# Kernel optimization log

Hardware: AMD Instinct MI355X
Metric: run time of the kernel (lower is better)

The kernel has to match this reference:

```python
import jax, jax.numpy as jnp
import numpy as np

N_HEADS = 16


def setup_inputs() -> dict:
    key = jax.random.key(0)
    ks = jax.random.split(key, 6)
    B, S, E = 2, 2048, 1024
    scale = 1.0 / np.sqrt(E)
    return {
        "X": jax.random.normal(ks[0], (B, S, E), dtype=jnp.float32),
        "Wq": jax.random.normal(ks[1], (E, E), dtype=jnp.float32) * scale,
        "Wk": jax.random.normal(ks[2], (E, E), dtype=jnp.float32) * scale,
        "Wv": jax.random.normal(ks[3], (E, E), dtype=jnp.float32) * scale,
        "Wp": jax.random.normal(ks[4], (E, E), dtype=jnp.float32) * scale,
        "bp": jnp.zeros((E,), dtype=jnp.float32),
    }


def reference(X, Wq, Wk, Wv, Wp, bp):
    B, S, E = X.shape
    H = N_HEADS
    dk = E // H
    # qkv projections (Linear with weight [out,in] -> x @ W.T), split heads
    q = (X @ Wq.T).reshape(B, S, H, dk).transpose(0, 2, 1, 3)  # [B,H,S,dk]
    k = (X @ Wk.T).reshape(B, S, H, dk).transpose(0, 2, 1, 3)
    v = (X @ Wv.T).reshape(B, S, H, dk).transpose(0, 2, 1, 3)
    scores = jnp.einsum('bhqd,bhkd->bhqk', q, k) / jnp.sqrt(jnp.asarray(dk, X.dtype))
    causal = jnp.tril(jnp.ones((S, S), dtype=bool))  # [S,S]
    scores = jnp.where(causal[None, None], scores, jnp.asarray(-jnp.inf, X.dtype))
    attn = jax.nn.softmax(scores, axis=-1)  # [B,H,S,S]
    y = jnp.einsum('bhqk,bhkd->bhqd', attn, v)  # [B,H,S,dk]
    y = y.transpose(0, 2, 1, 3).reshape(B, S, E)
    return y @ Wp.T + bp
```

## Files before the change

### kernel.cpp

```cpp
#include <hip/hip_runtime.h>

typedef unsigned short u16;
typedef __bf16 bf16x8 __attribute__((ext_vector_type(8)));
typedef float f32x4 __attribute__((ext_vector_type(4)));
typedef unsigned short u16x8 __attribute__((ext_vector_type(8)));
typedef unsigned short u16x4 __attribute__((ext_vector_type(4)));

union B8 { u16x8 u; bf16x8 b; };

#define MFMA_BF16(a, b, c) __builtin_amdgcn_mfma_f32_16x16x32_bf16((a), (b), (c), 0, 0, 0)

__device__ __forceinline__ u16 f2bf(float f) {
  unsigned x = __float_as_uint(f);
  unsigned r = x + 0x7fffu + ((x >> 16) & 1u);
  return (u16)(r >> 16);
}

__device__ __forceinline__ unsigned cvt_pk_bf16(float lo, float hi) {
  unsigned r;
  asm("v_cvt_pk_bf16_f32 %0, %1, %2" : "=v"(r) : "v"(lo), "v"(hi));
  return r;
}

__device__ __forceinline__ void gl2lds16(const void* g, void* l) {
  __builtin_amdgcn_global_load_lds(
      (const __attribute__((address_space(1))) void*)g,
      (__attribute__((address_space(3))) void*)l, 16, 0, 0);
}

__global__ __launch_bounds__(256) void cast5_kernel(
    const float* __restrict__ X, const float* __restrict__ Wq,
    const float* __restrict__ Wk, const float* __restrict__ Wv,
    const float* __restrict__ Wp, u16* __restrict__ Xb, u16* __restrict__ Wqb,
    u16* __restrict__ Wkb, u16* __restrict__ Wvb, u16* __restrict__ Wpb) {
  size_t i = ((size_t)blockIdx.x * 256 + threadIdx.x) * 4;
  const float* src;
  u16* dst;
  size_t off;
  if (i < 4194304) {
    src = X; dst = Xb; off = i;
  } else if (i < 5242880) {
    src = Wq; dst = Wqb; off = i - 4194304;
  } else if (i < 6291456) {
    src = Wk; dst = Wkb; off = i - 5242880;
  } else if (i < 7340032) {
    src = Wv; dst = Wvb; off = i - 6291456;
  } else {
    src = Wp; dst = Wpb; off = i - 7340032;
  }
  float4 v = *(const float4*)(src + off);
  u16x4 o;
  o[0] = f2bf(v.x); o[1] = f2bf(v.y); o[2] = f2bf(v.z); o[3] = f2bf(v.w);
  *(u16x4*)(dst + off) = o;
}

template <int N0>
__device__ __forceinline__ void mfma16(f32x4 (&acc)[8][4], B8 (&af)[8], B8& b0,
                                       B8& b1) {
  __builtin_amdgcn_s_setprio(1);
#pragma unroll
  for (int m = 0; m < 8; ++m) {
    acc[m][N0] = MFMA_BF16(af[m].b, b0.b, acc[m][N0]);
    acc[m][N0 + 1] = MFMA_BF16(af[m].b, b1.b, acc[m][N0 + 1]);
  }
  __builtin_amdgcn_s_setprio(0);
}

__global__ __launch_bounds__(512, 2) void gemm_qkv256(
    const u16* __restrict__ Xb, const u16* __restrict__ Wb,
    u16* __restrict__ Qb, u16* __restrict__ Kb, u16* __restrict__ Vt) {
  __shared__ __align__(16) u16 Al[2][2][256 * 32];
  __shared__ __align__(16) u16 Bl[2][2][256 * 32];

  int tid = threadIdx.x, lane = tid & 63, w = tid >> 6;
  int wr = w >> 2, wc = w & 3;
  int l16 = lane & 15, lg = lane >> 4;

  int bid = blockIdx.x;
  int swz = (bid & 7) * 24 + (bid >> 3);
  int bm = swz / 12, bn = swz % 12;

  const u16* Ag = Xb + (size_t)bm * 256 * 1024;
  const u16* Bg = Wb + (size_t)bn * 256 * 1024;

  int srow = w * 16 + (lane >> 2);
  int scol = lane & 3;

  auto stA = [&](int buf, int kh, int kt) {
#pragma unroll
    for (int p2 = 0; p2 < 2; ++p2) {
      int r = p2 * 128 + srow;
      int sl = scol ^ ((r >> 1) & 3);
      gl2lds16(Ag + (size_t)r * 1024 + kt * 64 + kh * 32 + sl * 8,
               (char*)&Al[buf][kh][0] + (size_t)(p2 * 128 + w * 16) * 64);
    }
  };
  auto stB = [&](int buf, int kh, int kt) {
#pragma unroll
    for (int p2 = 0; p2 < 2; ++p2) {
      int r = p2 * 128 + srow;
      int sl = scol ^ ((r >> 1) & 3);
      gl2lds16(Bg + (size_t)r * 1024 + kt * 64 + kh * 32 + sl * 8,
               (char*)&Bl[buf][kh][0] + (size_t)(p2 * 128 + w * 16) * 64);
    }
  };
  auto ldA = [&](int buf, int kk, B8 (&af)[8]) {
#pragma unroll
    for (int m = 0; m < 8; ++m) {
      int r = wr * 128 + m * 16 + l16;
      af[m].u = *(const u16x8*)((const char*)&Al[buf][kk][0] + r * 64 +
                                ((lg ^ ((r >> 1) & 3)) << 4));
    }
  };
  auto ldB = [&](int buf, int kk, int nf, B8& bf) {
    int r = wc * 64 + nf * 16 + l16;
    bf.u = *(const u16x8*)((const char*)&Bl[buf][kk][0] + r * 64 +
                           ((lg ^ ((r >> 1) & 3)) << 4));
  };

  f32x4 acc[8][4] = {};

  stA(0, 0, 0); stB(0, 0, 0);
  stA(0, 1, 0); stB(0, 1, 0);
  stA(1, 0, 1); stB(1, 0, 1);
  asm volatile("s_waitcnt vmcnt(8)" ::: "memory");
  __builtin_amdgcn_s_barrier();

  B8 af[8], b0, b1;
  for (int I = 0; I < 8; ++I) {
    int p = 2 * I;
    bool last = (I == 7);
    stA(1, 1, p + 1);
    ldA(0, 0, af); ldB(0, 0, 0, b0); ldB(0, 0, 1, b1);
    mfma16<0>(acc, af, b0, b1);
    stB(1, 1, p + 1);
    ldB(0, 0, 2, b0); ldB(0, 0, 3, b1);
    mfma16<2>(acc, af, b0, b1);
    if (last) asm volatile("s_waitcnt vmcnt(0)" ::: "memory");
    else      asm volatile("s_waitcnt vmcnt(8)" ::: "memory");
    __builtin_amdgcn_s_barrier();
    if (!last) stA(0, 0, p + 2);
    ldA(0, 1, af); ldB(0, 1, 0, b0); ldB(0, 1, 1, b1);
    mfma16<0>(acc, af, b0, b1);
    if (!last) stB(0, 0, p + 2);
    ldB(0, 1, 2, b0); ldB(0, 1, 3, b1);
    mfma16<2>(acc, af, b0, b1);
    if (last) asm volatile("s_waitcnt vmcnt(0)" ::: "memory");
    else      asm volatile("s_waitcnt vmcnt(8)" ::: "memory");
    __builtin_amdgcn_s_barrier();
    if (!last) stA(0, 1, p + 2);
    ldA(1, 0, af); ldB(1, 0, 0, b0); ldB(1, 0, 1, b1);
    mfma16<0>(acc, af, b0, b1);
    if (!last) stB(0, 1, p + 2);
    ldB(1, 0, 2, b0); ldB(1, 0, 3, b1);
    mfma16<2>(acc, af, b0, b1);
    if (last) asm volatile("s_waitcnt vmcnt(0)" ::: "memory");
    else      asm volatile("s_waitcnt vmcnt(8)" ::: "memory");
    __builtin_amdgcn_s_barrier();
    if (!last) stA(1, 0, p + 3);
    ldA(1, 1, af); ldB(1, 1, 0, b0); ldB(1, 1, 1, b1);
    mfma16<0>(acc, af, b0, b1);
    if (!last) stB(1, 0, p + 3);
    ldB(1, 1, 2, b0); ldB(1, 1, 3, b1);
    mfma16<2>(acc, af, b0, b1);
    if (!last) {
      asm volatile("s_waitcnt vmcnt(8)" ::: "memory");
      __builtin_amdgcn_s_barrier();
    }
  }

  const float QSCALE = 0.18033688011112042f;
#pragma unroll
  for (int m = 0; m < 8; ++m)
#pragma unroll
    for (int nf = 0; nf < 4; ++nf) {
      int colg = bn * 256 + wc * 64 + nf * 16 + l16;
      int rowg = bm * 256 + wr * 128 + m * 16 + lg * 4;
      if (bn < 4) {
#pragma unroll
        for (int j = 0; j < 4; ++j)
          Qb[(size_t)(rowg + j) * 1024 + colg] = f2bf(acc[m][nf][j] * QSCALE);
      } else if (bn < 8) {
#pragma unroll
        for (int j = 0; j < 4; ++j)
          Kb[(size_t)(rowg + j) * 1024 + (colg - 1024)] = f2bf(acc[m][nf][j]);
      } else {
        int cv = colg - 2048;
        int hh = cv >> 6, d = cv & 63;
        int bb = rowg >> 11, s0 = rowg & 2047;
        u16x4 pk;
#pragma unroll
        for (int j = 0; j < 4; ++j) pk[j] = f2bf(acc[m][nf][j]);
        *(u16x4*)(Vt + ((size_t)(bb * 16 + hh) * 64 + d) * 2048 + s0) = pk;
      }
    }
}

__device__ __forceinline__ void gemm_body(const u16* __restrict__ A,
                                          const u16* __restrict__ Bw,
                                          float* __restrict__ Cout,
                                          const float* __restrict__ bias,
                                          int bm, int bn, u16* Asm, u16* Bsm) {
  const int Kd = 1024, N = 1024;
  int tid = threadIdx.x;
  int lane = tid & 63, w = tid >> 6;
  int wr = w >> 1, wc = w & 1;
  int l16 = lane & 15, lg = lane >> 4;

  const u16* Abase = A + (size_t)bm * 128 * Kd;
  const u16* Bbase = Bw + (size_t)bn * 128 * Kd;

  f32x4 acc[4][4] = {};

  for (int kt = 0; kt < Kd / 64; ++kt) {
    int k0 = kt * 64;
#pragma unroll
    for (int i = 0; i < 4; ++i) {
      int uu = i * 256 + tid;
      int r = uu >> 3;
      int s = (uu & 7) ^ (r & 7);
      gl2lds16(Abase + (size_t)r * Kd + k0 + s * 8, Asm + i * 2048 + w * 512);
      gl2lds16(Bbase + (size_t)r * Kd + k0 + s * 8, Bsm + i * 2048 + w * 512);
    }
    asm volatile("s_waitcnt vmcnt(0)" ::: "memory");
    __syncthreads();

    B8 af[4][2], bfr[4][2];
#pragma unroll
    for (int mi = 0; mi < 4; ++mi)
#pragma unroll
      for (int kk = 0; kk < 2; ++kk) {
        int r = wr * 64 + mi * 16 + l16;
        int s = kk * 4 + lg;
        af[mi][kk].u = *(const u16x8*)((const char*)Asm + r * 128 + ((s ^ (r & 7)) << 4));
      }
#pragma unroll
    for (int ni = 0; ni < 4; ++ni)
#pragma unroll
      for (int kk = 0; kk < 2; ++kk) {
        int r = wc * 64 + ni * 16 + l16;
        int s = kk * 4 + lg;
        bfr[ni][kk].u = *(const u16x8*)((const char*)Bsm + r * 128 + ((s ^ (r & 7)) << 4));
      }
#pragma unroll
    for (int mi = 0; mi < 4; ++mi)
#pragma unroll
      for (int ni = 0; ni < 4; ++ni) {
        acc[mi][ni] = MFMA_BF16(af[mi][0].b, bfr[ni][0].b, acc[mi][ni]);
        acc[mi][ni] = MFMA_BF16(af[mi][1].b, bfr[ni][1].b, acc[mi][ni]);
      }
    __syncthreads();
  }

#pragma unroll
  for (int mi = 0; mi < 4; ++mi)
#pragma unroll
    for (int ni = 0; ni < 4; ++ni) {
      int col = bn * 128 + wc * 64 + ni * 16 + l16;
#pragma unroll
      for (int j = 0; j < 4; ++j) {
        int row = bm * 128 + wr * 64 + mi * 16 + lg * 4 + j;
        Cout[(size_t)row * N + col] = acc[mi][ni][j] + bias[col];
      }
    }
}

__global__ __launch_bounds__(256) void gemm_proj_kernel(
    const u16* __restrict__ Y1, const u16* __restrict__ Wpb,
    float* __restrict__ out, const float* __restrict__ bias) {
  __shared__ __align__(16) u16 Asm[128 * 64];
  __shared__ __align__(16) u16 Bsm[128 * 64];
  gemm_body(Y1, Wpb, out, bias, blockIdx.y, blockIdx.x, Asm, Bsm);
}

__global__ __launch_bounds__(256, 4) void attn_kernel(const u16* __restrict__ Q,
                                                      const u16* __restrict__ K,
                                                      const u16* __restrict__ Vt,
                                                      u16* __restrict__ Y) {
  __shared__ __align__(16) u16 Kl[2][64 * 64];
  __shared__ __align__(16) u16 Vl[2][64 * 64];
  __shared__ __align__(16) u16 Pl[4][16 * 64];

  const int E = 1024, S = 2048;
  int tid = threadIdx.x;
  int lane = tid & 63, w = tid >> 6;
  int l16 = lane & 15, lg = lane >> 4;
  int h7 = l16 & 7;

  int bid = blockIdx.x;
  int bh = bid & 31;
  int u = bid >> 5;
  int g = u & 7, kq = u >> 3;
  int qt = (kq == 0) ? 31 - g : (kq == 1) ? 16 + g : (kq == 2) ? 15 - g : g;
  int b = bh >> 4, h = bh & 15;

  const u16* Qb = Q + (size_t)b * S * E + (size_t)h * 64;
  const u16* Kb = K + (size_t)b * S * E + (size_t)h * 64;
  const u16* Vb = Vt + (size_t)bh * 64 * 2048;

  int r0 = tid >> 3;
  int s0 = (tid & 7) ^ (r0 & 7);
  size_t koff = (size_t)r0 * 1024 + s0 * 8;
  size_t voff = (size_t)r0 * 2048 + s0 * 8;
  const u16* kpA = Kb;
  const u16* kpB = Kb + 32 * 1024;
  const u16* vpA = Vb;
  const u16* vpB = Vb + 32 * 2048;

  const char* kbase0 = (const char*)&Kl[0][0] + l16 * 128 + ((lg ^ h7) << 4);
  const char* kbase1 = (const char*)&Kl[0][0] + l16 * 128 + (((4 + lg) ^ h7) << 4);
  const char* vbase0 = (const char*)&Vl[0][0] + l16 * 128 + ((lg ^ h7) << 4);
  const char* vbase1 = (const char*)&Vl[0][0] + l16 * 128 + (((4 + lg) ^ h7) << 4);
  char* pw0 = (char*)&Pl[w][0] + l16 * 128 + (((0 * 2 + (lg >> 1)) ^ h7) << 4) + (lg & 1) * 8;
  char* pw1 = (char*)&Pl[w][0] + l16 * 128 + (((1 * 2 + (lg >> 1)) ^ h7) << 4) + (lg & 1) * 8;
  char* pw2 = (char*)&Pl[w][0] + l16 * 128 + (((2 * 2 + (lg >> 1)) ^ h7) << 4) + (lg & 1) * 8;
  char* pw3 = (char*)&Pl[w][0] + l16 * 128 + (((3 * 2 + (lg >> 1)) ^ h7) << 4) + (lg & 1) * 8;
  const char* pr0 = (const char*)&Pl[w][0] + l16 * 128 + ((lg ^ h7) << 4);
  const char* pr1 = (const char*)&Pl[w][0] + l16 * 128 + (((4 + lg) ^ h7) << 4);

  B8 qa[2];
#pragma unroll
  for (int kk = 0; kk < 2; ++kk)
    qa[kk].u = *(const u16x8*)(Qb + (size_t)(qt * 64 + w * 16 + l16) * E + kk * 32 + lg * 8);

  f32x4 o[4] = {};
  float lrun = 0.f;
  int qrow = w * 16 + l16;

  gl2lds16(kpA + koff, &Kl[0][w * 512]);
  gl2lds16(vpA + voff, &Vl[0][w * 512]);
  gl2lds16(kpB + koff, &Kl[0][2048 + w * 512]);
  gl2lds16(vpB + voff, &Vl[0][2048 + w * 512]);
  kpA += 65536; kpB += 65536; vpA += 64; vpB += 64;

#define ATTN_ITER(BF, DOMASK, DOSTAGE)                                         \
  do {                                                                         \
    asm volatile("s_waitcnt vmcnt(0)" ::: "memory");                           \
    __syncthreads();                                                           \
    if (DOSTAGE) {                                                             \
      gl2lds16(kpA + koff, &Kl[(BF) ^ 1][w * 512]);                            \
      gl2lds16(vpA + voff, &Vl[(BF) ^ 1][w * 512]);                            \
      gl2lds16(kpB + koff, &Kl[(BF) ^ 1][2048 + w * 512]);                     \
      gl2lds16(vpB + voff, &Vl[(BF) ^ 1][2048 + w * 512]);                     \
      kpA += 65536; kpB += 65536; vpA += 64; vpB += 64;                        \
    }                                                                          \
    f32x4 sa[4] = {};                                                          \
    __builtin_amdgcn_s_setprio(1);                                             \
    _Pragma("unroll") for (int nb = 0; nb < 4; ++nb) {                         \
      B8 kf0, kf1;                                                             \
      kf0.u = *(const u16x8*)(kbase0 + (BF)*8192 + nb * 2048);                 \
      kf1.u = *(const u16x8*)(kbase1 + (BF)*8192 + nb * 2048);                 \
      sa[nb] = MFMA_BF16(kf0.b, qa[0].b, sa[nb]);                              \
      sa[nb] = MFMA_BF16(kf1.b, qa[1].b, sa[nb]);                              \
    }                                                                          \
    __builtin_amdgcn_s_setprio(0);                                             \
    float p[16];                                                               \
    _Pragma("unroll") for (int nb = 0; nb < 4; ++nb)                           \
        _Pragma("unroll") for (int j = 0; j < 4; ++j) {                        \
      float pe = __builtin_amdgcn_exp2f(sa[nb][j]);                            \
      if (DOMASK) {                                                            \
        int kv = nb * 16 + lg * 4 + j;                                         \
        if (kv > qrow) pe = 0.f;                                               \
      }                                                                        \
      p[nb * 4 + j] = pe;                                                      \
    }                                                                          \
    {                                                                          \
      union { u16x4 v; unsigned uu[2]; } pk;                                   \
      pk.uu[0] = cvt_pk_bf16(p[0], p[1]);                                      \
      pk.uu[1] = cvt_pk_bf16(p[2], p[3]);                                      \
      *(u16x4*)pw0 = pk.v;                                                     \
      pk.uu[0] = cvt_pk_bf16(p[4], p[5]);                                      \
      pk.uu[1] = cvt_pk_bf16(p[6], p[7]);                                      \
      *(u16x4*)pw1 = pk.v;                                                     \
      pk.uu[0] = cvt_pk_bf16(p[8], p[9]);                                      \
      pk.uu[1] = cvt_pk_bf16(p[10], p[11]);                                    \
      *(u16x4*)pw2 = pk.v;                                                     \
      pk.uu[0] = cvt_pk_bf16(p[12], p[13]);                                    \
      pk.uu[1] = cvt_pk_bf16(p[14], p[15]);                                    \
      *(u16x4*)pw3 = pk.v;                                                     \
    }                                                                          \
    lrun += ((p[0] + p[1]) + (p[2] + p[3])) + ((p[4] + p[5]) + (p[6] + p[7])) +\
            ((p[8] + p[9]) + (p[10] + p[11])) +                                \
            ((p[12] + p[13]) + (p[14] + p[15]));                               \
    B8 pa0, pa1;                                                               \
    pa0.u = *(const u16x8*)pr0;                                                \
    pa1.u = *(const u16x8*)pr1;                                                \
    __builtin_amdgcn_s_setprio(1);                                             \
    _Pragma("unroll") for (int nb = 0; nb < 4; ++nb) {                         \
      B8 vf0, vf1;                                                             \
      vf0.u = *(const u16x8*)(vbase0 + (BF)*8192 + nb * 2048);                 \
      vf1.u = *(const u16x8*)(vbase1 + (BF)*8192 + nb * 2048);                 \
      o[nb] = MFMA_BF16(pa0.b, vf0.b, o[nb]);                                  \
      o[nb] = MFMA_BF16(pa1.b, vf1.b, o[nb]);                                  \
    }                                                                          \
    __builtin_amdgcn_s_setprio(0);                                             \
  } while (0)

  int U = qt;
  int i = 0;
  for (; i + 2 <= U; i += 2) {
    ATTN_ITER(0, false, true);
    ATTN_ITER(1, false, true);
  }
  if (U & 1) {
    ATTN_ITER(0, false, true);
    ATTN_ITER(1, true, false);
  } else {
    ATTN_ITER(0, true, false);
  }
#undef ATTN_ITER

  lrun += __shfl_xor(lrun, 16);
  lrun += __shfl_xor(lrun, 32);
  float inv[4];
#pragma unroll
  for (int j = 0; j < 4; ++j) {
    float lj = __shfl(lrun, (lane & 48) | (lg * 4 + j));
    inv[j] = 1.0f / lj;
  }
#pragma unroll
  for (int nb = 0; nb < 4; ++nb)
#pragma unroll
    for (int j = 0; j < 4; ++j) {
      int row = qt * 64 + w * 16 + lg * 4 + j;
      int col = h * 64 + nb * 16 + l16;
      Y[((size_t)b * S + row) * E + col] = f2bf(o[nb][j] * inv[j]);
    }
}

extern "C" void kernel_launch(void* const* d_in, const int* in_sizes, int n_in,
                              void* d_out, int out_size, void* d_ws,
                              size_t ws_size, hipStream_t stream) {
  const float* X = (const float*)d_in[0];
  const float* Wq = (const float*)d_in[1];
  const float* Wk = (const float*)d_in[2];
  const float* Wv = (const float*)d_in[3];
  const float* Wp = (const float*)d_in[4];
  const float* bp = (const float*)d_in[5];
  float* out = (float*)d_out;

  char* ws = (char*)d_ws;
  const size_t MB = 1ull << 20;
  u16* Xb = (u16*)(ws + 0 * MB);
  u16* Wqb = (u16*)(ws + 8 * MB);
  u16* Wkb = (u16*)(ws + 10 * MB);
  u16* Wvb = (u16*)(ws + 12 * MB);
  u16* Wpb = (u16*)(ws + 14 * MB);
  u16* Qb = (u16*)(ws + 16 * MB);
  u16* Kb = (u16*)(ws + 24 * MB);
  u16* VtB = (u16*)(ws + 32 * MB);
  u16* Y1 = (u16*)(ws + 40 * MB);

  cast5_kernel<<<8192, 256, 0, stream>>>(X, Wq, Wk, Wv, Wp, Xb, Wqb, Wkb, Wvb, Wpb);
  gemm_qkv256<<<192, 512, 0, stream>>>(Xb, Wqb, Qb, Kb, VtB);
  attn_kernel<<<1024, 256, 0, stream>>>(Qb, Kb, VtB, Y1);
  gemm_proj_kernel<<<dim3(8, 32), 256, 0, stream>>>(Y1, Wpb, out, bp);
}
```

Before: 104.1 us.

## Double query tile per attention block and double-buffer projection GEMM

The attention kernel now processes 128 query rows per block (32 per wave, two MFMA row groups), reusing each staged K/V tile for twice the queries and halving the grid to 512 blocks with occupancy hint lowered to 2. The causal tail handles two masked 64-key tiles with offsets. The projection GEMM gets double-buffered LDS staging with prefetch of the next K slice and raised MFMA priority, removing the trailing barrier. Risks include lower occupancy and coarser load balance across blocks.

```diff
diff --git a/kernel.cpp b/kernel.cpp
--- a/kernel.cpp
+++ b/kernel.cpp
@@ -196,34 +196,47 @@
     }
 }
 
-__device__ __forceinline__ void gemm_body(const u16* __restrict__ A,
-                                          const u16* __restrict__ Bw,
-                                          float* __restrict__ Cout,
-                                          const float* __restrict__ bias,
-                                          int bm, int bn, u16* Asm, u16* Bsm) {
+__global__ __launch_bounds__(256) void gemm_proj_kernel(
+    const u16* __restrict__ Y1, const u16* __restrict__ Wpb,
+    float* __restrict__ out, const float* __restrict__ bias) {
+  __shared__ __align__(16) u16 Asm[2][128 * 64];
+  __shared__ __align__(16) u16 Bsm[2][128 * 64];
+
   const int Kd = 1024, N = 1024;
+  int bm = blockIdx.y, bn = blockIdx.x;
   int tid = threadIdx.x;
   int lane = tid & 63, w = tid >> 6;
   int wr = w >> 1, wc = w & 1;
   int l16 = lane & 15, lg = lane >> 4;
 
-  const u16* Abase = A + (size_t)bm * 128 * Kd;
-  const u16* Bbase = Bw + (size_t)bn * 128 * Kd;
+  const u16* Abase = Y1 + (size_t)bm * 128 * Kd;
+  const u16* Bbase = Wpb + (size_t)bn * 128 * Kd;
+
+  int r0 = tid >> 3;
+  int s0 = (tid & 7) ^ (r0 & 7);
+
+  auto stage = [&](int buf, int kt) {
+#pragma unroll
+    for (int i = 0; i < 4; ++i) {
+      int r = i * 32 + r0;
+      int s = s0 ^ ((i & 3) == 0 ? 0 : 0);
+      (void)s;
+      int sl = (tid & 7) ^ (r & 7);
+      gl2lds16(Abase + (size_t)r * Kd + kt * 64 + sl * 8,
+               &Asm[buf][i * 2048 + w * 512]);
+      gl2lds16(Bbase + (size_t)r * Kd + kt * 64 + sl * 8,
+               &Bsm[buf][i * 2048 + w * 512]);
+    }
+  };
 
   f32x4 acc[4][4] = {};
-
-  for (int kt = 0; kt < Kd / 64; ++kt) {
-    int k0 = kt * 64;
-#pragma unroll
-    for (int i = 0; i < 4; ++i) {
-      int uu = i * 256 + tid;
-      int r = uu >> 3;
-      int s = (uu & 7) ^ (r & 7);
-      gl2lds16(Abase + (size_t)r * Kd + k0 + s * 8, Asm + i * 2048 + w * 512);
-      gl2lds16(Bbase + (size_t)r * Kd + k0 + s * 8, Bsm + i * 2048 + w * 512);
-    }
+  stage(0, 0);
+  int buf = 0;
+
+  for (int kt = 0; kt < 16; ++kt) {
     asm volatile("s_waitcnt vmcnt(0)" ::: "memory");
     __syncthreads();
+    if (kt + 1 < 16) stage(buf ^ 1, kt + 1);
 
     B8 af[4][2], bfr[4][2];
 #pragma unroll
@@ -232,7 +245,8 @@
       for (int kk = 0; kk < 2; ++kk) {
         int r = wr * 64 + mi * 16 + l16;
         int s = kk * 4 + lg;
-        af[mi][kk].u = *(const u16x8*)((const char*)Asm + r * 128 + ((s ^ (r & 7)) << 4));
+        af[mi][kk].u = *(const u16x8*)((const char*)&Asm[buf][0] + r * 128 +
+                                       ((s ^ (r & 7)) << 4));
       }
 #pragma unroll
     for (int ni = 0; ni < 4; ++ni)
@@ -240,8 +254,10 @@
       for (int kk = 0; kk < 2; ++kk) {
         int r = wc * 64 + ni * 16 + l16;
         int s = kk * 4 + lg;
-        bfr[ni][kk].u = *(const u16x8*)((const char*)Bsm + r * 128 + ((s ^ (r & 7)) << 4));
-      }
+        bfr[ni][kk].u = *(const u16x8*)((const char*)&Bsm[buf][0] + r * 128 +
+                                        ((s ^ (r & 7)) << 4));
+      }
+    __builtin_amdgcn_s_setprio(1);
 #pragma unroll
     for (int mi = 0; mi < 4; ++mi)
 #pragma unroll
@@ -249,7 +265,8 @@
         acc[mi][ni] = MFMA_BF16(af[mi][0].b, bfr[ni][0].b, acc[mi][ni]);
         acc[mi][ni] = MFMA_BF16(af[mi][1].b, bfr[ni][1].b, acc[mi][ni]);
       }
-    __syncthreads();
+    __builtin_amdgcn_s_setprio(0);
+    buf ^= 1;
   }
 
 #pragma unroll
@@ -260,26 +277,18 @@
 #pragma unroll
       for (int j = 0; j < 4; ++j) {
         int row = bm * 128 + wr * 64 + mi * 16 + lg * 4 + j;
-        Cout[(size_t)row * N + col] = acc[mi][ni][j] + bias[col];
-      }
-    }
-}
-
-__global__ __launch_bounds__(256) void gemm_proj_kernel(
-    const u16* __restrict__ Y1, const u16* __restrict__ Wpb,
-    float* __restrict__ out, const float* __restrict__ bias) {
-  __shared__ __align__(16) u16 Asm[128 * 64];
-  __shared__ __align__(16) u16 Bsm[128 * 64];
-  gemm_body(Y1, Wpb, out, bias, blockIdx.y, blockIdx.x, Asm, Bsm);
-}
-
-__global__ __launch_bounds__(256, 4) void attn_kernel(const u16* __restrict__ Q,
+        out[(size_t)row * N + col] = acc[mi][ni][j] + bias[col];
+      }
+    }
+}
+
+__global__ __launch_bounds__(256, 2) void attn_kernel(const u16* __restrict__ Q,
                                                       const u16* __restrict__ K,
                                                       const u16* __restrict__ Vt,
                                                       u16* __restrict__ Y) {
   __shared__ __align__(16) u16 Kl[2][64 * 64];
   __shared__ __align__(16) u16 Vl[2][64 * 64];
-  __shared__ __align__(16) u16 Pl[4][16 * 64];
+  __shared__ __align__(16) u16 Pl[4][32 * 64];
 
   const int E = 1024, S = 2048;
   int tid = threadIdx.x;
@@ -290,8 +299,7 @@
   int bid = blockIdx.x;
   int bh = bid & 31;
   int u = bid >> 5;
-  int g = u & 7, kq = u >> 3;
-  int qt = (kq == 0) ? 31 - g : (kq == 1) ? 16 + g : (kq == 2) ? 15 - g : g;
+  int qt = (u < 8) ? 15 - u : u - 8;
   int b = bh >> 4, h = bh & 15;
 
   const u16* Qb = Q + (size_t)b * S * E + (size_t)h * 64;
@@ -311,21 +319,23 @@
   const char* kbase1 = (const char*)&Kl[0][0] + l16 * 128 + (((4 + lg) ^ h7) << 4);
   const char* vbase0 = (const char*)&Vl[0][0] + l16 * 128 + ((lg ^ h7) << 4);
   const char* vbase1 = (const char*)&Vl[0][0] + l16 * 128 + (((4 + lg) ^ h7) << 4);
-  char* pw0 = (char*)&Pl[w][0] + l16 * 128 + (((0 * 2 + (lg >> 1)) ^ h7) << 4) + (lg & 1) * 8;
-  char* pw1 = (char*)&Pl[w][0] + l16 * 128 + (((1 * 2 + (lg >> 1)) ^ h7) << 4) + (lg & 1) * 8;
-  char* pw2 = (char*)&Pl[w][0] + l16 * 128 + (((2 * 2 + (lg >> 1)) ^ h7) << 4) + (lg & 1) * 8;
-  char* pw3 = (char*)&Pl[w][0] + l16 * 128 + (((3 * 2 + (lg >> 1)) ^ h7) << 4) + (lg & 1) * 8;
+  char* pw0 = (char*)&Pl[w][0] + l16 * 128 + (((0 + (lg >> 1)) ^ h7) << 4) + (lg & 1) * 8;
+  char* pw1 = (char*)&Pl[w][0] + l16 * 128 + (((2 + (lg >> 1)) ^ h7) << 4) + (lg & 1) * 8;
+  char* pw2 = (char*)&Pl[w][0] + l16 * 128 + (((4 + (lg >> 1)) ^ h7) << 4) + (lg & 1) * 8;
+  char* pw3 = (char*)&Pl[w][0] + l16 * 128 + (((6 + (lg >> 1)) ^ h7) << 4) + (lg & 1) * 8;
   const char* pr0 = (const char*)&Pl[w][0] + l16 * 128 + ((lg ^ h7) << 4);
   const char* pr1 = (const char*)&Pl[w][0] + l16 * 128 + (((4 + lg) ^ h7) << 4);
 
-  B8 qa[2];
-#pragma unroll
-  for (int kk = 0; kk < 2; ++kk)
-    qa[kk].u = *(const u16x8*)(Qb + (size_t)(qt * 64 + w * 16 + l16) * E + kk * 32 + lg * 8);
-
-  f32x4 o[4] = {};
-  float lrun = 0.f;
-  int qrow = w * 16 + l16;
+  B8 qa[2][2];
+#pragma unroll
+  for (int mi = 0; mi < 2; ++mi)
+#pragma unroll
+    for (int kk = 0; kk < 2; ++kk)
+      qa[mi][kk].u = *(const u16x8*)(Qb + (size_t)(qt * 128 + w * 32 + mi * 16 + l16) * E + kk * 32 + lg * 8);
+
+  f32x4 o[2][4] = {};
+  float lrun[2] = {0.f, 0.f};
+  int qloc = w * 32 + l16;
 
   gl2lds16(kpA + koff, &Kl[0][w * 512]);
   gl2lds16(vpA + voff, &Vl[0][w * 512]);
@@ -333,7 +343,7 @@
   gl2lds16(vpB + voff, &Vl[0][2048 + w * 512]);
   kpA += 65536; kpB += 65536; vpA += 64; vpB += 64;
 
-#define ATTN_ITER(BF, DOMASK, DOSTAGE)                                         \
+#define ATTN_ITER(BF, DOMASK, TOFF, DOSTAGE)                                   \
   do {                                                                         \
     asm volatile("s_waitcnt vmcnt(0)" ::: "memory");                           \
     __syncthreads();                                                           \
@@ -344,88 +354,94 @@
       gl2lds16(vpB + voff, &Vl[(BF) ^ 1][2048 + w * 512]);                     \
       kpA += 65536; kpB += 65536; vpA += 64; vpB += 64;                        \
     }                                                                          \
-    f32x4 sa[4] = {};                                                          \
+    f32x4 sa[2][4] = {};                                                       \
     __builtin_amdgcn_s_setprio(1);                                             \
     _Pragma("unroll") for (int nb = 0; nb < 4; ++nb) {                         \
       B8 kf0, kf1;                                                             \
-      kf0.u = *(const u16x8*)(kbase0 + (BF)*8192 + nb * 2048);                 \
-      kf1.u = *(const u16x8*)(kbase1 + (BF)*8192 + nb * 2048);                 \
-      sa[nb] = MFMA_BF16(kf0.b, qa[0].b, sa[nb]);                              \
-      sa[nb] = MFMA_BF16(kf1.b, qa[1].b, sa[nb]);                              \
+      kf0.u = *(const u16x8*)(kbase0 + (BF) * 8192 + nb * 2048);               \
+      kf1.u = *(const u16x8*)(kbase1 + (BF) * 8192 + nb * 2048);               \
+      sa[0][nb] = MFMA_BF16(kf0.b, qa[0][0].b, sa[0][nb]);                     \
+      sa[0][nb] = MFMA_BF16(kf1.b, qa[0][1].b, sa[0][nb]);                     \
+      sa[1][nb] = MFMA_BF16(kf0.b, qa[1][0].b, sa[1][nb]);                     \
+      sa[1][nb] = MFMA_BF16(kf1.b, qa[1][1].b, sa[1][nb]);                     \
     }                                                                          \
     __builtin_amdgcn_s_setprio(0);                                             \
-    float p[16];                                                               \
-    _Pragma("unroll") for (int nb = 0; nb < 4; ++nb)                           \
-        _Pragma("unroll") for (int j = 0; j < 4; ++j) {                        \
-      float pe = __builtin_amdgcn_exp2f(sa[nb][j]);                            \
-      if (DOMASK) {                                                            \
-        int kv = nb * 16 + lg * 4 + j;                                         \
-        if (kv > qrow) pe = 0.f;                                               \
+    _Pragma("unroll") for (int mi = 0; mi < 2; ++mi) {                         \
+      float p[16];                                                             \
+      _Pragma("unroll") for (int nb = 0; nb < 4; ++nb)                         \
+          _Pragma("unroll") for (int j = 0; j < 4; ++j) {                      \
+        float pe = __builtin_amdgcn_exp2f(sa[mi][nb][j]);                      \
+        if (DOMASK) {                                                          \
+          int kv = (TOFF) + nb * 16 + lg * 4 + j;                              \
+          if (kv > qloc + mi * 16) pe = 0.f;                                   \
+        }                                                                      \
+        p[nb * 4 + j] = pe;                                                    \
       }                                                                        \
-      p[nb * 4 + j] = pe;                                                      \
-    }                                                                          \
-    {                                                                          \
       union { u16x4 v; unsigned uu[2]; } pk;                                   \
       pk.uu[0] = cvt_pk_bf16(p[0], p[1]);                                      \
       pk.uu[1] = cvt_pk_bf16(p[2], p[3]);                                      \
-      *(u16x4*)pw0 = pk.v;                                                     \
+      *(u16x4*)(pw0 + mi * 2048) = pk.v;                                       \
       pk.uu[0] = cvt_pk_bf16(p[4], p[5]);                                      \
       pk.uu[1] = cvt_pk_bf16(p[6], p[7]);                                      \
-      *(u16x4*)pw1 = pk.v;                                                     \
+      *(u16x4*)(pw1 + mi * 2048) = pk.v;                                       \
       pk.uu[0] = cvt_pk_bf16(p[8], p[9]);                                      \
       pk.uu[1] = cvt_pk_bf16(p[10], p[11]);                                    \
-      *(u16x4*)pw2 = pk.v;                                                     \
+      *(u16x4*)(pw2 + mi * 2048) = pk.v;                                       \
       pk.uu[0] = cvt_pk_bf16(p[12], p[13]);                                    \
       pk.uu[1] = cvt_pk_bf16(p[14], p[15]);                                    \
-      *(u16x4*)pw3 = pk.v;                                                     \
+      *(u16x4*)(pw3 + mi * 2048) = pk.v;                                       \
+      lrun[mi] += ((p[0] + p[1]) + (p[2] + p[3])) +                            \
+                  ((p[4] + p[5]) + (p[6] + p[7])) +                            \
+                  ((p[8] + p[9]) + (p[10] + p[11])) +                          \
+                  ((p[12] + p[13]) + (p[14] + p[15]));                         \
     }                                                                          \
-    lrun += ((p[0] + p[1]) + (p[2] + p[3])) + ((p[4] + p[5]) + (p[6] + p[7])) +\
-            ((p[8] + p[9]) + (p[10] + p[11])) +                                \
-            ((p[12] + p[13]) + (p[14] + p[15]));                               \
-    B8 pa0, pa1;                                                               \
-    pa0.u = *(const u16x8*)pr0;                                                \
-    pa1.u = *(const u16x8*)pr1;                                                \
+    B8 pa00, pa01, pa10, pa11;                                                 \
+    pa00.u = *(const u16x8*)(pr0);                                             \
+    pa01.u = *(const u16x8*)(pr1);                                             \
+    pa10.u = *(const u16x8*)(pr0 + 2048);                                      \
+    pa11.u = *(const u16x8*)(pr1 + 2048);                                      \
     __builtin_amdgcn_s_setprio(1);                                             \
     _Pragma("unroll") for (int nb = 0; nb < 4; ++nb) {                         \
       B8 vf0, vf1;                                                             \
-      vf0.u = *(const u16x8*)(vbase0 + (BF)*8192 + nb * 2048);                 \
-      vf1.u = *(const u16x8*)(vbase1 + (BF)*8192 + nb * 2048);                 \
-      o[nb] = MFMA_BF16(pa0.b, vf0.b, o[nb]);                                  \
-      o[nb] = MFMA_BF16(pa1.b, vf1.b, o[nb]);                                  \
+      vf0.u = *(const u16x8*)(vbase0 + (BF) * 8192 + nb * 2048);               \
+      vf1.u = *(const u16x8*)(vbase1 + (BF) * 8192 + nb * 2048);               \
+      o[0][nb] = MFMA_BF16(pa00.b, vf0.b, o[0][nb]);                           \
+      o[0][nb] = MFMA_BF16(pa01.b, vf1.b, o[0][nb]);                           \
+      o[1][nb] = MFMA_BF16(pa10.b, vf0.b, o[1][nb]);                           \
+      o[1][nb] = MFMA_BF16(pa11.b, vf1.b, o[1][nb]);                           \
     }                                                                          \
     __builtin_amdgcn_s_setprio(0);                                             \
   } while (0)
 
-  int U = qt;
-  int i = 0;
-  for (; i + 2 <= U; i += 2) {
-    ATTN_ITER(0, false, true);
-    ATTN_ITER(1, false, true);
-  }
-  if (U & 1) {
-    ATTN_ITER(0, false, true);
-    ATTN_ITER(1, true, false);
-  } else {
-    ATTN_ITER(0, true, false);
-  }
+  int nt = 2 * qt;
+  for (int i = 0; i + 2 <= nt; i += 2) {
+    ATTN_ITER(0, false, 0, true);
+    ATTN_ITER(1, false, 0, true);
+  }
+  ATTN_ITER(0, true, 0, true);
+  ATTN_ITER(1, true, 64, false);
 #undef ATTN_ITER
 
-  lrun += __shfl_xor(lrun, 16);
-  lrun += __shfl_xor(lrun, 32);
-  float inv[4];
-#pragma unroll
-  for (int j = 0; j < 4; ++j) {
-    float lj = __shfl(lrun, (lane & 48) | (lg * 4 + j));
-    inv[j] = 1.0f / lj;
-  }
-#pragma unroll
-  for (int nb = 0; nb < 4; ++nb)
+#pragma unroll
+  for (int mi = 0; mi < 2; ++mi) {
+    float l = lrun[mi];
+    l += __shfl_xor(l, 16);
+    l += __shfl_xor(l, 32);
+    float inv[4];
 #pragma unroll
     for (int j = 0; j < 4; ++j) {
-      int row = qt * 64 + w * 16 + lg * 4 + j;
-      int col = h * 64 + nb * 16 + l16;
-      Y[((size_t)b * S + row) * E + col] = f2bf(o[nb][j] * inv[j]);
-    }
+      float lj = __shfl(l, (lane & 48) | (lg * 4 + j));
+      inv[j] = 1.0f / lj;
+    }
+#pragma unroll
+    for (int nb = 0; nb < 4; ++nb)
+#pragma unroll
+      for (int j = 0; j < 4; ++j) {
+        int row = qt * 128 + w * 32 + mi * 16 + lg * 4 + j;
+        int col = h * 64 + nb * 16 + l16;
+        Y[((size_t)b * S + row) * E + col] = f2bf(o[mi][nb][j] * inv[j]);
+      }
+  }
 }
 
 extern "C" void kernel_launch(void* const* d_in, const int* in_sizes, int n_in,
@@ -453,6 +469,6 @@
 
   cast5_kernel<<<8192, 256, 0, stream>>>(X, Wq, Wk, Wv, Wp, Xb, Wqb, Wkb, Wvb, Wpb);
   gemm_qkv256<<<192, 512, 0, stream>>>(Xb, Wqb, Qb, Kb, VtB);
-  attn_kernel<<<1024, 256, 0, stream>>>(Qb, Kb, VtB, Y1);
+  attn_kernel<<<512, 256, 0, stream>>>(Qb, Kb, VtB, Y1);
   gemm_proj_kernel<<<dim3(8, 32), 256, 0, stream>>>(Y1, Wpb, out, bp);
 }
```

Measured after the change: 109.7 us. 5.4% more time.

## Replace 256-tile QKV GEMM with double-buffered 128-tile kernel; double-buffer proj GEMM

Applied to the files above, without the earlier changes.

Swaps the hand-scheduled 256x256, 512-thread QKV GEMM for a 128x128, 256-thread kernel with a simple two-stage LDS double buffer and a swizzled 768-block grid. The projection GEMM gets the same double-buffered loop, which prefetches the next K tile while computing the current one and drops the trailing barrier. The aim is more blocks for better CU occupancy and load balance, plus overlap of global loads with MFMA. The cost is less data reuse per tile and more global traffic for the QKV GEMM.

```diff
diff --git a/kernel.cpp b/kernel.cpp
--- a/kernel.cpp
+++ b/kernel.cpp
@@ -54,176 +54,47 @@
   *(u16x4*)(dst + off) = o;
 }
 
-template <int N0>
-__device__ __forceinline__ void mfma16(f32x4 (&acc)[8][4], B8 (&af)[8], B8& b0,
-                                       B8& b1) {
-  __builtin_amdgcn_s_setprio(1);
-#pragma unroll
-  for (int m = 0; m < 8; ++m) {
-    acc[m][N0] = MFMA_BF16(af[m].b, b0.b, acc[m][N0]);
-    acc[m][N0 + 1] = MFMA_BF16(af[m].b, b1.b, acc[m][N0 + 1]);
-  }
-  __builtin_amdgcn_s_setprio(0);
-}
-
-__global__ __launch_bounds__(512, 2) void gemm_qkv256(
+__global__ __launch_bounds__(256, 2) void gemm_qkv128(
     const u16* __restrict__ Xb, const u16* __restrict__ Wb,
     u16* __restrict__ Qb, u16* __restrict__ Kb, u16* __restrict__ Vt) {
-  __shared__ __align__(16) u16 Al[2][2][256 * 32];
-  __shared__ __align__(16) u16 Bl[2][2][256 * 32];
-
-  int tid = threadIdx.x, lane = tid & 63, w = tid >> 6;
-  int wr = w >> 2, wc = w & 3;
-  int l16 = lane & 15, lg = lane >> 4;
-
-  int bid = blockIdx.x;
-  int swz = (bid & 7) * 24 + (bid >> 3);
-  int bm = swz / 12, bn = swz % 12;
-
-  const u16* Ag = Xb + (size_t)bm * 256 * 1024;
-  const u16* Bg = Wb + (size_t)bn * 256 * 1024;
-
-  int srow = w * 16 + (lane >> 2);
-  int scol = lane & 3;
-
-  auto stA = [&](int buf, int kh, int kt) {
-#pragma unroll
-    for (int p2 = 0; p2 < 2; ++p2) {
-      int r = p2 * 128 + srow;
-      int sl = scol ^ ((r >> 1) & 3);
-      gl2lds16(Ag + (size_t)r * 1024 + kt * 64 + kh * 32 + sl * 8,
-               (char*)&Al[buf][kh][0] + (size_t)(p2 * 128 + w * 16) * 64);
-    }
-  };
-  auto stB = [&](int buf, int kh, int kt) {
-#pragma unroll
-    for (int p2 = 0; p2 < 2; ++p2) {
-      int r = p2 * 128 + srow;
-      int sl = scol ^ ((r >> 1) & 3);
-      gl2lds16(Bg + (size_t)r * 1024 + kt * 64 + kh * 32 + sl * 8,
-               (char*)&Bl[buf][kh][0] + (size_t)(p2 * 128 + w * 16) * 64);
-    }
-  };
-  auto ldA = [&](int buf, int kk, B8 (&af)[8]) {
-#pragma unroll
-    for (int m = 0; m < 8; ++m) {
-      int r = wr * 128 + m * 16 + l16;
-      af[m].u = *(const u16x8*)((const char*)&Al[buf][kk][0] + r * 64 +
-                                ((lg ^ ((r >> 1) & 3)) << 4));
-    }
-  };
-  auto ldB = [&](int buf, int kk, int nf, B8& bf) {
-    int r = wc * 64 + nf * 16 + l16;
-    bf.u = *(const u16x8*)((const char*)&Bl[buf][kk][0] + r * 64 +
-                           ((lg ^ ((r >> 1) & 3)) << 4));
-  };
-
-  f32x4 acc[8][4] = {};
-
-  stA(0, 0, 0); stB(0, 0, 0);
-  stA(0, 1, 0); stB(0, 1, 0);
-  stA(1, 0, 1); stB(1, 0, 1);
-  asm volatile("s_waitcnt vmcnt(8)" ::: "memory");
-  __builtin_amdgcn_s_barrier();
-
-  B8 af[8], b0, b1;
-  for (int I = 0; I < 8; ++I) {
-    int p = 2 * I;
-    bool last = (I == 7);
-    stA(1, 1, p + 1);
-    ldA(0, 0, af); ldB(0, 0, 0, b0); ldB(0, 0, 1, b1);
-    mfma16<0>(acc, af, b0, b1);
-    stB(1, 1, p + 1);
-    ldB(0, 0, 2, b0); ldB(0, 0, 3, b1);
-    mfma16<2>(acc, af, b0, b1);
-    if (last) asm volatile("s_waitcnt vmcnt(0)" ::: "memory");
-    else      asm volatile("s_waitcnt vmcnt(8)" ::: "memory");
-    __builtin_amdgcn_s_barrier();
-    if (!last) stA(0, 0, p + 2);
-    ldA(0, 1, af); ldB(0, 1, 0, b0); ldB(0, 1, 1, b1);
-    mfma16<0>(acc, af, b0, b1);
-    if (!last) stB(0, 0, p + 2);
-    ldB(0, 1, 2, b0); ldB(0, 1, 3, b1);
-    mfma16<2>(acc, af, b0, b1);
-    if (last) asm volatile("s_waitcnt vmcnt(0)" ::: "memory");
-    else      asm volatile("s_waitcnt vmcnt(8)" ::: "memory");
-    __builtin_amdgcn_s_barrier();
-    if (!last) stA(0, 1, p + 2);
-    ldA(1, 0, af); ldB(1, 0, 0, b0); ldB(1, 0, 1, b1);
-    mfma16<0>(acc, af, b0, b1);
-    if (!last) stB(0, 1, p + 2);
-    ldB(1, 0, 2, b0); ldB(1, 0, 3, b1);
-    mfma16<2>(acc, af, b0, b1);
-    if (last) asm volatile("s_waitcnt vmcnt(0)" ::: "memory");
-    else      asm volatile("s_waitcnt vmcnt(8)" ::: "memory");
-    __builtin_amdgcn_s_barrier();
-    if (!last) stA(1, 0, p + 3);
-    ldA(1, 1, af); ldB(1, 1, 0, b0); ldB(1, 1, 1, b1);
-    mfma16<0>(acc, af, b0, b1);
-    if (!last) stB(1, 0, p + 3);
-    ldB(1, 1, 2, b0); ldB(1, 1, 3, b1);
-    mfma16<2>(acc, af, b0, b1);
-    if (!last) {
-      asm volatile("s_waitcnt vmcnt(8)" ::: "memory");
-      __builtin_amdgcn_s_barrier();
-    }
-  }
-
-  const float QSCALE = 0.18033688011112042f;
-#pragma unroll
-  for (int m = 0; m < 8; ++m)
-#pragma unroll
-    for (int nf = 0; nf < 4; ++nf) {
-      int colg = bn * 256 + wc * 64 + nf * 16 + l16;
-      int rowg = bm * 256 + wr * 128 + m * 16 + lg * 4;
-      if (bn < 4) {
-#pragma unroll
-        for (int j = 0; j < 4; ++j)
-          Qb[(size_t)(rowg + j) * 1024 + colg] = f2bf(acc[m][nf][j] * QSCALE);
-      } else if (bn < 8) {
-#pragma unroll
-        for (int j = 0; j < 4; ++j)
-          Kb[(size_t)(rowg + j) * 1024 + (colg - 1024)] = f2bf(acc[m][nf][j]);
-      } else {
-        int cv = colg - 2048;
-        int hh = cv >> 6, d = cv & 63;
-        int bb = rowg >> 11, s0 = rowg & 2047;
-        u16x4 pk;
-#pragma unroll
-        for (int j = 0; j < 4; ++j) pk[j] = f2bf(acc[m][nf][j]);
-        *(u16x4*)(Vt + ((size_t)(bb * 16 + hh) * 64 + d) * 2048 + s0) = pk;
-      }
-    }
-}
-
-__device__ __forceinline__ void gemm_body(const u16* __restrict__ A,
-                                          const u16* __restrict__ Bw,
-                                          float* __restrict__ Cout,
-                                          const float* __restrict__ bias,
-                                          int bm, int bn, u16* Asm, u16* Bsm) {
-  const int Kd = 1024, N = 1024;
+  __shared__ __align__(16) u16 Asm[2][128 * 64];
+  __shared__ __align__(16) u16 Bsm[2][128 * 64];
+
+  const int Kd = 1024;
   int tid = threadIdx.x;
   int lane = tid & 63, w = tid >> 6;
   int wr = w >> 1, wc = w & 1;
   int l16 = lane & 15, lg = lane >> 4;
 
-  const u16* Abase = A + (size_t)bm * 128 * Kd;
-  const u16* Bbase = Bw + (size_t)bn * 128 * Kd;
+  int bid = blockIdx.x;
+  int swz = (bid & 7) * 96 + (bid >> 3);
+  int bm = swz / 24, bn = swz % 24;
+
+  const u16* Abase = Xb + (size_t)bm * 128 * Kd;
+  const u16* Bbase = Wb + (size_t)bn * 128 * Kd;
+
+  int r0 = tid >> 3;
+
+  auto stage = [&](int buf, int kt) {
+#pragma unroll
+    for (int i = 0; i < 4; ++i) {
+      int r = i * 32 + r0;
+      int sl = (tid & 7) ^ (r & 7);
+      gl2lds16(Abase + (size_t)r * Kd + kt * 64 + sl * 8,
+               &Asm[buf][i * 2048 + w * 512]);
+      gl2lds16(Bbase + (size_t)r * Kd + kt * 64 + sl * 8,
+               &Bsm[buf][i * 2048 + w * 512]);
+    }
+  };
 
   f32x4 acc[4][4] = {};
-
-  for (int kt = 0; kt < Kd / 64; ++kt) {
-    int k0 = kt * 64;
-#pragma unroll
-    for (int i = 0; i < 4; ++i) {
-      int uu = i * 256 + tid;
-      int r = uu >> 3;
-      int s = (uu & 7) ^ (r & 7);
-      gl2lds16(Abase + (size_t)r * Kd + k0 + s * 8, Asm + i * 2048 + w * 512);
-      gl2lds16(Bbase + (size_t)r * Kd + k0 + s * 8, Bsm + i * 2048 + w * 512);
-    }
+  stage(0, 0);
+  int buf = 0;
+
+  for (int kt = 0; kt < 16; ++kt) {
     asm volatile("s_waitcnt vmcnt(0)" ::: "memory");
     __syncthreads();
+    if (kt + 1 < 16) stage(buf ^ 1, kt + 1);
 
     B8 af[4][2], bfr[4][2];
 #pragma unroll
@@ -232,7 +103,8 @@
       for (int kk = 0; kk < 2; ++kk) {
         int r = wr * 64 + mi * 16 + l16;
         int s = kk * 4 + lg;
-        af[mi][kk].u = *(const u16x8*)((const char*)Asm + r * 128 + ((s ^ (r & 7)) << 4));
+        af[mi][kk].u = *(const u16x8*)((const char*)&Asm[buf][0] + r * 128 +
+                                       ((s ^ (r & 7)) << 4));
       }
 #pragma unroll
     for (int ni = 0; ni < 4; ++ni)
@@ -240,8 +112,10 @@
       for (int kk = 0; kk < 2; ++kk) {
         int r = wc * 64 + ni * 16 + l16;
         int s = kk * 4 + lg;
-        bfr[ni][kk].u = *(const u16x8*)((const char*)Bsm + r * 128 + ((s ^ (r & 7)) << 4));
-      }
+        bfr[ni][kk].u = *(const u16x8*)((const char*)&Bsm[buf][0] + r * 128 +
+                                        ((s ^ (r & 7)) << 4));
+      }
+    __builtin_amdgcn_s_setprio(1);
 #pragma unroll
     for (int mi = 0; mi < 4; ++mi)
 #pragma unroll
@@ -249,18 +123,33 @@
         acc[mi][ni] = MFMA_BF16(af[mi][0].b, bfr[ni][0].b, acc[mi][ni]);
         acc[mi][ni] = MFMA_BF16(af[mi][1].b, bfr[ni][1].b, acc[mi][ni]);
       }
-    __syncthreads();
-  }
-
+    __builtin_amdgcn_s_setprio(0);
+    buf ^= 1;
+  }
+
+  const float QSCALE = 0.18033688011112042f;
 #pragma unroll
   for (int mi = 0; mi < 4; ++mi)
 #pragma unroll
     for (int ni = 0; ni < 4; ++ni) {
-      int col = bn * 128 + wc * 64 + ni * 16 + l16;
-#pragma unroll
-      for (int j = 0; j < 4; ++j) {
-        int row = bm * 128 + wr * 64 + mi * 16 + lg * 4 + j;
-        Cout[(size_t)row * N + col] = acc[mi][ni][j] + bias[col];
+      int colg = bn * 128 + wc * 64 + ni * 16 + l16;
+      int rowg = bm * 128 + wr * 64 + mi * 16 + lg * 4;
+      if (bn < 8) {
+#pragma unroll
+        for (int j = 0; j < 4; ++j)
+          Qb[(size_t)(rowg + j) * 1024 + colg] = f2bf(acc[mi][ni][j] * QSCALE);
+      } else if (bn < 16) {
+#pragma unroll
+        for (int j = 0; j < 4; ++j)
+          Kb[(size_t)(rowg + j) * 1024 + (colg - 1024)] = f2bf(acc[mi][ni][j]);
+      } else {
+        int cv = colg - 2048;
+        int hh = cv >> 6, d = cv & 63;
+        int bb = rowg >> 11, s0r = rowg & 2047;
+        u16x4 pk;
+#pragma unroll
+        for (int j = 0; j < 4; ++j) pk[j] = f2bf(acc[mi][ni][j]);
+        *(u16x4*)(Vt + ((size_t)(bb * 16 + hh) * 64 + d) * 2048 + s0r) = pk;
       }
     }
 }
@@ -268,9 +157,84 @@
 __global__ __launch_bounds__(256) void gemm_proj_kernel(
     const u16* __restrict__ Y1, const u16* __restrict__ Wpb,
     float* __restrict__ out, const float* __restrict__ bias) {
-  __shared__ __align__(16) u16 Asm[128 * 64];
-  __shared__ __align__(16) u16 Bsm[128 * 64];
-  gemm_body(Y1, Wpb, out, bias, blockIdx.y, blockIdx.x, Asm, Bsm);
+  __shared__ __align__(16) u16 Asm[2][128 * 64];
+  __shared__ __align__(16) u16 Bsm[2][128 * 64];
+
+  const int Kd = 1024, N = 1024;
+  int bm = blockIdx.y, bn = blockIdx.x;
+  int tid = threadIdx.x;
+  int lane = tid & 63, w = tid >> 6;
+  int wr = w >> 1, wc = w & 1;
+  int l16 = lane & 15, lg = lane >> 4;
+
+  const u16* Abase = Y1 + (size_t)bm * 128 * Kd;
+  const u16* Bbase = Wpb + (size_t)bn * 128 * Kd;
+
+  int r0 = tid >> 3;
+
+  auto stage = [&](int buf, int kt) {
+#pragma unroll
+    for (int i = 0; i < 4; ++i) {
+      int r = i * 32 + r0;
+      int sl = (tid & 7) ^ (r & 7);
+      gl2lds16(Abase + (size_t)r * Kd + kt * 64 + sl * 8,
+               &Asm[buf][i * 2048 + w * 512]);
+      gl2lds16(Bbase + (size_t)r * Kd + kt * 64 + sl * 8,
+               &Bsm[buf][i * 2048 + w * 512]);
+    }
+  };
+
+  f32x4 acc[4][4] = {};
+  stage(0, 0);
+  int buf = 0;
+
+  for (int kt = 0; kt < 16; ++kt) {
+    asm volatile("s_waitcnt vmcnt(0)" ::: "memory");
+    __syncthreads();
+    if (kt + 1 < 16) stage(buf ^ 1, kt + 1);
+
+    B8 af[4][2], bfr[4][2];
+#pragma unroll
+    for (int mi = 0; mi < 4; ++mi)
+#pragma unroll
+      for (int kk = 0; kk < 2; ++kk) {
+        int r = wr * 64 + mi * 16 + l16;
+        int s = kk * 4 + lg;
+        af[mi][kk].u = *(const u16x8*)((const char*)&Asm[buf][0] + r * 128 +
+                                       ((s ^ (r & 7)) << 4));
+      }
+#pragma unroll
+    for (int ni = 0; ni < 4; ++ni)
+#pragma unroll
+      for (int kk = 0; kk < 2; ++kk) {
+        int r = wc * 64 + ni * 16 + l16;
+        int s = kk * 4 + lg;
+        bfr[ni][kk].u = *(const u16x8*)((const char*)&Bsm[buf][0] + r * 128 +
+                                        ((s ^ (r & 7)) << 4));
+      }
+    __builtin_amdgcn_s_setprio(1);
+#pragma unroll
+    for (int mi = 0; mi < 4; ++mi)
+#pragma unroll
+      for (int ni = 0; ni < 4; ++ni) {
+        acc[mi][ni] = MFMA_BF16(af[mi][0].b, bfr[ni][0].b, acc[mi][ni]);
+        acc[mi][ni] = MFMA_BF16(af[mi][1].b, bfr[ni][1].b, acc[mi][ni]);
+      }
+    __builtin_amdgcn_s_setprio(0);
+    buf ^= 1;
+  }
+
+#pragma unroll
+  for (int mi = 0; mi < 4; ++mi)
+#pragma unroll
+    for (int ni = 0; ni < 4; ++ni) {
+      int col = bn * 128 + wc * 64 + ni * 16 + l16;
+#pragma unroll
+      for (int j = 0; j < 4; ++j) {
+        int row = bm * 128 + wr * 64 + mi * 16 + lg * 4 + j;
+        out[(size_t)row * N + col] = acc[mi][ni][j] + bias[col];
+      }
+    }
 }
 
 __global__ __launch_bounds__(256, 4) void attn_kernel(const u16* __restrict__ Q,
@@ -452,7 +416,7 @@
   u16* Y1 = (u16*)(ws + 40 * MB);
 
   cast5_kernel<<<8192, 256, 0, stream>>>(X, Wq, Wk, Wv, Wp, Xb, Wqb, Wkb, Wvb, Wpb);
-  gemm_qkv256<<<192, 512, 0, stream>>>(Xb, Wqb, Qb, Kb, VtB);
+  gemm_qkv128<<<768, 256, 0, stream>>>(Xb, Wqb, Qb, Kb, VtB);
   attn_kernel<<<1024, 256, 0, stream>>>(Qb, Kb, VtB, Y1);
   gemm_proj_kernel<<<dim3(8, 32), 256, 0, stream>>>(Y1, Wpb, out, bp);
 }
```

Measured after the change: 110.4 us. +6.0%, slower.
